# Kernel tuning notes

Hardware: AMD Instinct MI355X
Metric: run time of the kernel (lower is better)

The kernel has to match this reference:

```python
import jax, jax.numpy as jnp
import numpy as np

D_MODEL = 1024
N_HEADS = 16
D_HEAD = D_MODEL // N_HEADS


def setup_inputs() -> dict:
    key = jax.random.key(0)
    k_x, k_wqkv, k_bqkv, k_wo, k_bo = jax.random.split(key, 5)
    B, T = 2, 2048
    scale = 1.0 / np.sqrt(D_MODEL)
    return {
        "x": jax.random.normal(k_x, (B, T, D_MODEL), dtype=jnp.float32),
        "w_qkv": jax.random.uniform(k_wqkv, (D_MODEL, 3 * D_MODEL), jnp.float32, -scale, scale),
        "b_qkv": jax.random.uniform(k_bqkv, (3 * D_MODEL,), jnp.float32, -scale, scale),
        "w_out": jax.random.uniform(k_wo, (D_MODEL, D_MODEL), jnp.float32, -scale, scale),
        "b_out": jax.random.uniform(k_bo, (D_MODEL,), jnp.float32, -scale, scale),
    }


def reference(x, w_qkv, b_qkv, w_out, b_out):
    B, T, D = x.shape
    qkv = x @ w_qkv + b_qkv                      # [B,T,3D]
    q, k, v = jnp.split(qkv, 3, axis=-1)
    # [B,T,D] -> [B,H,T,d]
    def split_heads(t):
        return t.reshape(B, T, N_HEADS, D_HEAD).transpose(0, 2, 1, 3)
    q, k, v = split_heads(q), split_heads(k), split_heads(v)
    scores = jnp.einsum('bhqd,bhkd->bhqk', q, k) / np.sqrt(D_HEAD)
    probs = jax.nn.softmax(scores, axis=-1)      # dropout p=0 (eval)
    out = jnp.einsum('bhqk,bhkd->bhqd', probs, v)
    out = out.transpose(0, 2, 1, 3).reshape(B, T, D)
    return out @ w_out + b_out
```

## Files before the change

kernel.cpp:

```cpp
#include <hip/hip_runtime.h>
#include <hip/hip_bf16.h>
#include <math.h>

#define D_MODEL 1024
#define N_HEADS 16
#define D_HEAD  64
#define SEQ     2048
#define NBATCH  2
#define NROWS   (NBATCH * SEQ)

#define C2F 0.18033688011112042f

typedef __attribute__((ext_vector_type(8))) short short8v;
typedef __attribute__((ext_vector_type(4))) float f32x4;
typedef __attribute__((ext_vector_type(16))) float f32x16;
typedef __attribute__((ext_vector_type(4))) unsigned int u32x4;

__device__ __forceinline__ unsigned short f2bf(float x) {
    unsigned int u = __float_as_uint(x);
    return (unsigned short)((u + 0x7FFFu + ((u >> 16) & 1u)) >> 16);
}
__device__ __forceinline__ void split_bf(float x, unsigned short& hi, unsigned short& lo) {
    unsigned int u = __float_as_uint(x);
    unsigned int ht = u & 0xFFFF0000u;
    hi = (unsigned short)(ht >> 16);
    lo = f2bf(x - __uint_as_float(ht));
}
__device__ __forceinline__ unsigned int cvtpk(float lo, float hi) {
    unsigned int r;
    asm("v_cvt_pk_bf16_f32 %0, %1, %2" : "=v"(r) : "v"(lo), "v"(hi));
    return r;
}
__device__ __forceinline__ short8v u2s(u32x4 v) {
    union { u32x4 u; short8v s; } c; c.u = v; return c.s;
}

__global__ __launch_bounds__(256) void splitT_kernel(
    const float* __restrict__ W, unsigned short* __restrict__ Th,
    unsigned short* __restrict__ Tl, int K, int N, int qcols, int write_lo)
{
    __shared__ float tile[64][68];
    const int tid = threadIdx.x;
    const int nbn = N >> 6;
    const int k0 = (blockIdx.x / nbn) << 6;
    const int n0 = (blockIdx.x % nbn) << 6;
    const int r  = tid >> 4;
    const int c4 = (tid & 15) * 4;

#pragma unroll
    for (int i = 0; i < 4; ++i) {
        float4 v = *(const float4*)(W + (size_t)(k0 + r + i * 16) * N + n0 + c4);
        *(float4*)&tile[r + i * 16][c4] = v;
    }
    __syncthreads();

    const int kl = (tid & 15) * 4;
#pragma unroll
    for (int i = 0; i < 4; ++i) {
        const int nl = (tid >> 4) + i * 16;
        const float sc = (n0 + nl < qcols) ? C2F : 1.0f;
        if (write_lo) {
            ushort4 h4, l4;
            unsigned short h, l;
            split_bf(tile[kl + 0][nl] * sc, h, l); h4.x = h; l4.x = l;
            split_bf(tile[kl + 1][nl] * sc, h, l); h4.y = h; l4.y = l;
            split_bf(tile[kl + 2][nl] * sc, h, l); h4.z = h; l4.z = l;
            split_bf(tile[kl + 3][nl] * sc, h, l); h4.w = h; l4.w = l;
            *(ushort4*)(Th + (size_t)(n0 + nl) * K + k0 + kl) = h4;
            *(ushort4*)(Tl + (size_t)(n0 + nl) * K + k0 + kl) = l4;
        } else {
            ushort4 h4;
            h4.x = f2bf(tile[kl + 0][nl] * sc);
            h4.y = f2bf(tile[kl + 1][nl] * sc);
            h4.z = f2bf(tile[kl + 2][nl] * sc);
            h4.w = f2bf(tile[kl + 3][nl] * sc);
            *(ushort4*)(Th + (size_t)(n0 + nl) * K + k0 + kl) = h4;
        }
    }
}

#define ASTRIDE 40

__global__ __launch_bounds__(256) void gemm_xw_kernel(
    const float* __restrict__ A,
    const unsigned short* __restrict__ Bth,
    const float* __restrict__ bias,
    unsigned short* __restrict__ C, int M, int N, int K, int qcols)
{
    __shared__ __align__(16) unsigned short Ab[128][ASTRIDE];
    __shared__ __align__(16) unsigned short Bh[128][ASTRIDE];

    const int tid  = threadIdx.x;
    const int wave = tid >> 6;
    const int lane = tid & 63;
    const int col  = lane & 15;
    const int q4   = lane >> 4;
    const int wm   = (wave >> 1) * 64;
    const int wn   = (wave & 1) * 64;

    const int nwg = gridDim.x;
    const int cpx = nwg >> 3;
    const int swz = (blockIdx.x & 7) * cpx + (blockIdx.x >> 3);
    const int nbn = N / 128;
    const int bm = (swz / nbn) * 128;
    const int bn = (swz % nbn) * 128;

    const int sr = tid >> 1;
    const int sq = (tid & 1) * 16;
    const float* aptr = A + (size_t)(bm + sr) * K + sq;
    const unsigned short* bhp = Bth + (size_t)(bn + sr) * K + sq;

    f32x4 acc[4][4];
#pragma unroll
    for (int i = 0; i < 4; ++i)
#pragma unroll
        for (int j = 0; j < 4; ++j) acc[i][j] = (f32x4){0.f, 0.f, 0.f, 0.f};

    float4 a0, a1, a2, a3;
    short8v b0h, b1h;

#define G1LOAD(k0) { \
    a0 = *(const float4*)(aptr + (k0)); \
    a1 = *(const float4*)(aptr + (k0) + 4); \
    a2 = *(const float4*)(aptr + (k0) + 8); \
    a3 = *(const float4*)(aptr + (k0) + 12); \
    b0h = *(const short8v*)(bhp + (k0)); \
    b1h = *(const short8v*)(bhp + (k0) + 8); \
}

#define G1WRITE() { \
    u32x4 p0, p1; \
    p0.x = cvtpk(a0.x, a0.y); p0.y = cvtpk(a0.z, a0.w); \
    p0.z = cvtpk(a1.x, a1.y); p0.w = cvtpk(a1.z, a1.w); \
    p1.x = cvtpk(a2.x, a2.y); p1.y = cvtpk(a2.z, a2.w); \
    p1.z = cvtpk(a3.x, a3.y); p1.w = cvtpk(a3.z, a3.w); \
    *(u32x4*)&Ab[sr][sq]     = p0; \
    *(u32x4*)&Ab[sr][sq + 8] = p1; \
    *(short8v*)&Bh[sr][sq]     = b0h; \
    *(short8v*)&Bh[sr][sq + 8] = b1h; \
}

#define G1COMP() { \
    short8v af[4]; \
    _Pragma("unroll") \
    for (int mt = 0; mt < 4; ++mt) \
        af[mt] = *(const short8v*)&Ab[wm + mt * 16 + col][q4 * 8]; \
    _Pragma("unroll") \
    for (int nt = 0; nt < 4; ++nt) { \
        short8v bhf = *(const short8v*)&Bh[wn + nt * 16 + col][q4 * 8]; \
        _Pragma("unroll") \
        for (int mt = 0; mt < 4; ++mt) \
            acc[mt][nt] = __builtin_amdgcn_mfma_f32_16x16x32_bf16(af[mt], bhf, acc[mt][nt], 0, 0, 0); \
    } \
}

    G1LOAD(0);
    G1WRITE();
    for (int k0 = 32; k0 < K; k0 += 32) {
        G1LOAD(k0);
        __syncthreads();
        G1COMP();
        __syncthreads();
        G1WRITE();
    }
    __syncthreads();
    G1COMP();
#undef G1LOAD
#undef G1WRITE
#undef G1COMP

    const float bscale = (bn < qcols) ? C2F : 1.0f;
    float bv[4];
#pragma unroll
    for (int nt = 0; nt < 4; ++nt) bv[nt] = bias[bn + wn + nt * 16 + col] * bscale;

#pragma unroll
    for (int mt = 0; mt < 4; ++mt)
#pragma unroll
        for (int r = 0; r < 4; ++r) {
            const int row = bm + wm + mt * 16 + q4 * 4 + r;
#pragma unroll
            for (int nt = 0; nt < 4; ++nt)
                C[(size_t)row * N + bn + wn + nt * 16 + col] = f2bf(acc[mt][nt][r] + bv[nt]);
        }
}

__global__ __launch_bounds__(256) void gemm_ao_kernel(
    const unsigned short* __restrict__ Aoh,
    const unsigned short* __restrict__ Aol,
    const unsigned short* __restrict__ Bth,
    const unsigned short* __restrict__ Btl,
    const float* __restrict__ bias,
    float* __restrict__ C, int M, int N, int K)
{
    __shared__ __align__(16) unsigned short Ah[128][ASTRIDE];
    __shared__ __align__(16) unsigned short Al[128][ASTRIDE];
    __shared__ __align__(16) unsigned short Bh[128][ASTRIDE];
    __shared__ __align__(16) unsigned short Bl[128][ASTRIDE];

    const int tid  = threadIdx.x;
    const int wave = tid >> 6;
    const int lane = tid & 63;
    const int col  = lane & 15;
    const int q4   = lane >> 4;
    const int wm   = (wave >> 1) * 64;
    const int wn   = (wave & 1) * 64;

    const int nwg = gridDim.x;
    const int cpx = nwg >> 3;
    const int swz = (blockIdx.x & 7) * cpx + (blockIdx.x >> 3);
    const int nbn = N / 128;
    const int bm = (swz / nbn) * 128;
    const int bn = (swz % nbn) * 128;

    const int sr = tid >> 1;
    const int sq = (tid & 1) * 16;
    const unsigned short* ahp = Aoh + (size_t)(bm + sr) * K + sq;
    const unsigned short* alp = Aol + (size_t)(bm + sr) * K + sq;
    const unsigned short* bhp = Bth + (size_t)(bn + sr) * K + sq;
    const unsigned short* blp = Btl + (size_t)(bn + sr) * K + sq;

    f32x4 acc[4][4];
#pragma unroll
    for (int i = 0; i < 4; ++i)
#pragma unroll
        for (int j = 0; j < 4; ++j) acc[i][j] = (f32x4){0.f, 0.f, 0.f, 0.f};

    short8v a0h, a1h, a0l, a1l, b0h, b1h, b0l, b1l;

#define G2LOAD(k0) { \
    a0h = *(const short8v*)(ahp + (k0)); \
    a1h = *(const short8v*)(ahp + (k0) + 8); \
    a0l = *(const short8v*)(alp + (k0)); \
    a1l = *(const short8v*)(alp + (k0) + 8); \
    b0h = *(const short8v*)(bhp + (k0)); \
    b1h = *(const short8v*)(bhp + (k0) + 8); \
    b0l = *(const short8v*)(blp + (k0)); \
    b1l = *(const short8v*)(blp + (k0) + 8); \
}

#define G2WRITE() { \
    *(short8v*)&Ah[sr][sq]     = a0h; \
    *(short8v*)&Ah[sr][sq + 8] = a1h; \
    *(short8v*)&Al[sr][sq]     = a0l; \
    *(short8v*)&Al[sr][sq + 8] = a1l; \
    *(short8v*)&Bh[sr][sq]     = b0h; \
    *(short8v*)&Bh[sr][sq + 8] = b1h; \
    *(short8v*)&Bl[sr][sq]     = b0l; \
    *(short8v*)&Bl[sr][sq + 8] = b1l; \
}

#define G2COMP() { \
    short8v ahf[4], alf[4]; \
    _Pragma("unroll") \
    for (int mt = 0; mt < 4; ++mt) { \
        ahf[mt] = *(const short8v*)&Ah[wm + mt * 16 + col][q4 * 8]; \
        alf[mt] = *(const short8v*)&Al[wm + mt * 16 + col][q4 * 8]; \
    } \
    _Pragma("unroll") \
    for (int nt = 0; nt < 4; ++nt) { \
        short8v bhf = *(const short8v*)&Bh[wn + nt * 16 + col][q4 * 8]; \
        short8v blf = *(const short8v*)&Bl[wn + nt * 16 + col][q4 * 8]; \
        _Pragma("unroll") \
        for (int mt = 0; mt < 4; ++mt) { \
            acc[mt][nt] = __builtin_amdgcn_mfma_f32_16x16x32_bf16(ahf[mt], bhf, acc[mt][nt], 0, 0, 0); \
            acc[mt][nt] = __builtin_amdgcn_mfma_f32_16x16x32_bf16(alf[mt], bhf, acc[mt][nt], 0, 0, 0); \
            acc[mt][nt] = __builtin_amdgcn_mfma_f32_16x16x32_bf16(ahf[mt], blf, acc[mt][nt], 0, 0, 0); \
        } \
    } \
}

    G2LOAD(0);
    G2WRITE();
    for (int k0 = 32; k0 < K; k0 += 32) {
        G2LOAD(k0);
        __syncthreads();
        G2COMP();
        __syncthreads();
        G2WRITE();
    }
    __syncthreads();
    G2COMP();
#undef G2LOAD
#undef G2WRITE
#undef G2COMP

    float bv[4];
#pragma unroll
    for (int nt = 0; nt < 4; ++nt) bv[nt] = bias[bn + wn + nt * 16 + col];

#pragma unroll
    for (int mt = 0; mt < 4; ++mt)
#pragma unroll
        for (int r = 0; r < 4; ++r) {
            const int row = bm + wm + mt * 16 + q4 * 4 + r;
#pragma unroll
            for (int nt = 0; nt < 4; ++nt)
                C[(size_t)row * N + bn + wn + nt * 16 + col] = acc[mt][nt][r] + bv[nt];
        }
}

__global__ __launch_bounds__(256) void attn_mfma_kernel(
    const unsigned short* __restrict__ qkv,
    unsigned short* __restrict__ aoh, unsigned short* __restrict__ aol)
{
    __shared__ __align__(16) unsigned short Ks[64 * 64];
    __shared__ __align__(16) unsigned short Vt[64 * 64];

    const int tid  = threadIdx.x;
    const int wave = tid >> 6;
    const int lane = tid & 63;
    const int l31  = lane & 31;
    const int lh   = lane >> 5;

    const int bh = blockIdx.x;
    const int qt = blockIdx.y;
    const int b = bh >> 4;
    const int h = bh & 15;
    const int qrow0 = b * SEQ + qt * 128 + wave * 32;
    const int krow0 = b * SEQ;

    bool s1;
    {
        int ta = lane, tb = 4096 + lane;
        asm volatile("v_permlane32_swap_b32 %0, %1" : "+v"(ta), "+v"(tb));
        s1 = __all((lane < 32) ? (ta == lane) : (ta == 4096 + lane - 32));
    }

    short8v qf[4];
    {
        const unsigned short* qsrc = qkv + (size_t)(qrow0 + l31) * (3 * D_MODEL) + h * 64 + lh * 8;
#pragma unroll
        for (int s = 0; s < 4; ++s)
            qf[s] = *(const short8v*)(qsrc + s * 16);
    }

    const int krow = tid >> 2;
    const int koff = (tid & 3) * 16;
    const int vk0  = (tid & 31) * 2;
    const int vd0  = (tid >> 5) * 8;

    const unsigned short* kp = qkv + (size_t)(krow0 + krow) * (3 * D_MODEL)
                               + D_MODEL + h * 64 + koff;
    const unsigned short* vp = qkv + (size_t)(krow0 + vk0) * (3 * D_MODEL)
                               + 2 * D_MODEL + h * 64 + vd0;
    const ptrdiff_t CSTRIDE = (ptrdiff_t)64 * 3 * D_MODEL;

    f32x16 ot0, ot1;
#pragma unroll
    for (int r = 0; r < 16; ++r) { ot0[r] = 0.f; ot1[r] = 0.f; }
    float ll = 0.f;

    short8v kg[2], vg[2];
    const int swr = (l31 & 7) << 3;

#define PLSWAP(a, b) asm volatile("v_permlane32_swap_b32 %0, %1" : "+v"(a), "+v"(b))

#define ALOAD() { \
    kg[0] = ((const short8v*)kp)[0]; \
    kg[1] = ((const short8v*)kp)[1]; \
    vg[0] = *(const short8v*)(vp); \
    vg[1] = *(const short8v*)(vp + 3 * D_MODEL); \
    kp += CSTRIDE; vp += CSTRIDE; \
}

#define AWRITE() { \
    const int base = krow * 64 + koff; \
    const int sw = (krow & 7) << 3; \
    *(short8v*)&Ks[(base)     ^ sw] = kg[0]; \
    *(short8v*)&Ks[(base + 8) ^ sw] = kg[1]; \
    _Pragma("unroll") \
    for (int j = 0; j < 8; ++j) { \
        ushort2 w; \
        w.x = ((const unsigned short*)&vg[0])[j]; \
        w.y = ((const unsigned short*)&vg[1])[j]; \
        const int d = vd0 + j; \
        *(ushort2*)&Vt[(d * 64 + vk0) ^ ((d & 7) << 3)] = w; \
    } \
}

#define ACOMPUTE() { \
    f32x16 st0, st1; \
    _Pragma("unroll") for (int r = 0; r < 16; ++r) { st0[r] = 0.f; st1[r] = 0.f; } \
    _Pragma("unroll") \
    for (int s = 0; s < 4; ++s) { \
        short8v kf0 = *(const short8v*)&Ks[(l31 * 64 + s * 16 + lh * 8) ^ swr]; \
        st0 = __builtin_amdgcn_mfma_f32_32x32x16_bf16(kf0, qf[s], st0, 0, 0, 0); \
    } \
    _Pragma("unroll") \
    for (int s = 0; s < 4; ++s) { \
        short8v kf1 = *(const short8v*)&Ks[((32 + l31) * 64 + s * 16 + lh * 8) ^ swr]; \
        st1 = __builtin_amdgcn_mfma_f32_32x32x16_bf16(kf1, qf[s], st1, 0, 0, 0); \
    } \
    _Pragma("unroll") \
    for (int r = 0; r < 16; ++r) { \
        st0[r] = __builtin_exp2f(st0[r]); \
        st1[r] = __builtin_exp2f(st1[r]); \
    } \
    { \
        float a0 = (st0[0] + st0[1]) + (st0[2] + st0[3]); \
        float a1 = (st0[4] + st0[5]) + (st0[6] + st0[7]); \
        float a2 = (st0[8] + st0[9]) + (st0[10] + st0[11]); \
        float a3 = (st0[12] + st0[13]) + (st0[14] + st0[15]); \
        float b0 = (st1[0] + st1[1]) + (st1[2] + st1[3]); \
        float b1 = (st1[4] + st1[5]) + (st1[6] + st1[7]); \
        float b2 = (st1[8] + st1[9]) + (st1[10] + st1[11]); \
        float b3 = (st1[12] + st1[13]) + (st1[14] + st1[15]); \
        float rs = ((a0 + a1) + (a2 + a3)) + ((b0 + b1) + (b2 + b3)); \
        rs += __shfl_xor(rs, 32); \
        ll += rs; \
    } \
    unsigned int pk[16]; \
    _Pragma("unroll") \
    for (int i2 = 0; i2 < 8; ++i2) { \
        pk[i2]     = cvtpk(st0[2 * i2], st0[2 * i2 + 1]); \
        pk[8 + i2] = cvtpk(st1[2 * i2], st1[2 * i2 + 1]); \
    } \
    if (s1) { \
        PLSWAP(pk[0], pk[2]);   PLSWAP(pk[1], pk[3]); \
        PLSWAP(pk[4], pk[6]);   PLSWAP(pk[5], pk[7]); \
        PLSWAP(pk[8], pk[10]);  PLSWAP(pk[9], pk[11]); \
        PLSWAP(pk[12], pk[14]); PLSWAP(pk[13], pk[15]); \
    } else { \
        PLSWAP(pk[2], pk[0]);   PLSWAP(pk[3], pk[1]); \
        PLSWAP(pk[6], pk[4]);   PLSWAP(pk[7], pk[5]); \
        PLSWAP(pk[10], pk[8]);  PLSWAP(pk[11], pk[9]); \
        PLSWAP(pk[14], pk[12]); PLSWAP(pk[15], pk[13]); \
    } \
    u32x4 pf[4]; \
    pf[0].x = pk[0];  pf[0].y = pk[1];  pf[0].z = pk[2];  pf[0].w = pk[3]; \
    pf[1].x = pk[4];  pf[1].y = pk[5];  pf[1].z = pk[6];  pf[1].w = pk[7]; \
    pf[2].x = pk[8];  pf[2].y = pk[9];  pf[2].z = pk[10]; pf[2].w = pk[11]; \
    pf[3].x = pk[12]; pf[3].y = pk[13]; pf[3].z = pk[14]; pf[3].w = pk[15]; \
    _Pragma("unroll") \
    for (int ks2 = 0; ks2 < 4; ++ks2) { \
        const short8v pfr = u2s(pf[ks2]); \
        const int keyoff = ks2 * 16 + lh * 8; \
        short8v vf0 = *(const short8v*)&Vt[(l31 * 64 + keyoff) ^ swr]; \
        ot0 = __builtin_amdgcn_mfma_f32_32x32x16_bf16(vf0, pfr, ot0, 0, 0, 0); \
        short8v vf1 = *(const short8v*)&Vt[((32 + l31) * 64 + keyoff) ^ swr]; \
        ot1 = __builtin_amdgcn_mfma_f32_32x32x16_bf16(vf1, pfr, ot1, 0, 0, 0); \
    } \
}

    ALOAD();
    AWRITE();
    for (int i = 0; i < 31; ++i) {
        ALOAD();
        __syncthreads();
        ACOMPUTE();
        __syncthreads();
        AWRITE();
    }
    __syncthreads();
    ACOMPUTE();
#undef ALOAD
#undef AWRITE
#undef ACOMPUTE
#undef PLSWAP

    const float il = 1.0f / ll;
    const int qrow = qrow0 + l31;
    unsigned short* dh = aoh + (size_t)qrow * D_MODEL + h * 64;
    unsigned short* dl = aol + (size_t)qrow * D_MODEL + h * 64;
#pragma unroll
    for (int r = 0; r < 16; ++r) {
        const int dloc = (r & 3) + 8 * (r >> 2) + 4 * lh;
        unsigned short hh, lo2;
        split_bf(ot0[r] * il, hh, lo2);
        dh[dloc] = hh; dl[dloc] = lo2;
        split_bf(ot1[r] * il, hh, lo2);
        dh[32 + dloc] = hh; dl[32 + dloc] = lo2;
    }
}

extern "C" void kernel_launch(void* const* d_in, const int* in_sizes, int n_in,
                              void* d_out, int out_size, void* d_ws, size_t ws_size,
                              hipStream_t stream) {
    (void)in_sizes; (void)n_in; (void)out_size; (void)ws_size;

    const float* x     = (const float*)d_in[0];
    const float* w_qkv = (const float*)d_in[1];
    const float* b_qkv = (const float*)d_in[2];
    const float* w_out = (const float*)d_in[3];
    const float* b_out = (const float*)d_in[4];
    float* out = (float*)d_out;

    char* ws = (char*)d_ws;
    unsigned short* qkv_bf  = (unsigned short*)(ws);
    unsigned short* aoh     = (unsigned short*)(ws + 25165824);
    unsigned short* aol     = (unsigned short*)(ws + 33554432);
    unsigned short* wqkvT_h = (unsigned short*)(ws + 41943040);
    unsigned short* woutT_h = (unsigned short*)(ws + 48234496);
    unsigned short* woutT_l = (unsigned short*)(ws + 50331648);

    splitT_kernel<<<dim3((D_MODEL / 64) * (3 * D_MODEL / 64)), 256, 0, stream>>>(
        w_qkv, wqkvT_h, (unsigned short*)nullptr, D_MODEL, 3 * D_MODEL, D_MODEL, 0);
    splitT_kernel<<<dim3((D_MODEL / 64) * (D_MODEL / 64)), 256, 0, stream>>>(
        w_out, woutT_h, woutT_l, D_MODEL, D_MODEL, 0, 1);

    gemm_xw_kernel<<<dim3((NROWS / 128) * (3 * D_MODEL / 128)), 256, 0, stream>>>(
        x, wqkvT_h, b_qkv, qkv_bf, NROWS, 3 * D_MODEL, D_MODEL, D_MODEL);

    attn_mfma_kernel<<<dim3(NBATCH * N_HEADS, SEQ / 128), 256, 0, stream>>>(qkv_bf, aoh, aol);

    gemm_ao_kernel<<<dim3((NROWS / 128) * (D_MODEL / 128)), 256, 0, stream>>>(
        aoh, aol, woutT_h, woutT_l, b_out, out, NROWS, D_MODEL, D_MODEL);
}
```

Measured before the change: 155.7 us.

## Split attention over two key halves with a separate merge kernel

The attention kernel gains a third grid dimension that splits the 2048 keys into two halves. Each half writes unnormalized fp32 partial outputs and row sums to workspace, and a new merge kernel adds them, normalizes, and produces the bf16 hi/lo split. This doubles the block count to improve CU occupancy on the attention stage. In exchange it adds about 64MB of extra global traffic, one more launch, and workspace aliasing. The merge is only correct if both halves use the same softmax offset.

```diff
diff --git a/kernel.cpp b/kernel.cpp
--- a/kernel.cpp
+++ b/kernel.cpp
@@ -302,7 +302,8 @@
 
 __global__ __launch_bounds__(256) void attn_mfma_kernel(
     const unsigned short* __restrict__ qkv,
-    unsigned short* __restrict__ aoh, unsigned short* __restrict__ aol)
+    float* __restrict__ Op0, float* __restrict__ Op1,
+    float* __restrict__ l0, float* __restrict__ l1)
 {
     __shared__ __align__(16) unsigned short Ks[64 * 64];
     __shared__ __align__(16) unsigned short Vt[64 * 64];
@@ -315,10 +316,14 @@
 
     const int bh = blockIdx.x;
     const int qt = blockIdx.y;
+    const int ks = blockIdx.z;
     const int b = bh >> 4;
     const int h = bh & 15;
     const int qrow0 = b * SEQ + qt * 128 + wave * 32;
-    const int krow0 = b * SEQ;
+    const int krow0 = b * SEQ + ks * 1024;
+
+    float* __restrict__ Op = ks ? Op1 : Op0;
+    float* __restrict__ lb = ks ? l1 : l0;
 
     bool s1;
     {
@@ -445,7 +450,7 @@
 
     ALOAD();
     AWRITE();
-    for (int i = 0; i < 31; ++i) {
+    for (int i = 0; i < 15; ++i) {
         ALOAD();
         __syncthreads();
         ACOMPUTE();
@@ -459,19 +464,48 @@
 #undef ACOMPUTE
 #undef PLSWAP
 
-    const float il = 1.0f / ll;
     const int qrow = qrow0 + l31;
-    unsigned short* dh = aoh + (size_t)qrow * D_MODEL + h * 64;
-    unsigned short* dl = aol + (size_t)qrow * D_MODEL + h * 64;
+    float* dst = Op + (size_t)qrow * D_MODEL + h * 64;
 #pragma unroll
     for (int r = 0; r < 16; ++r) {
         const int dloc = (r & 3) + 8 * (r >> 2) + 4 * lh;
-        unsigned short hh, lo2;
-        split_bf(ot0[r] * il, hh, lo2);
-        dh[dloc] = hh; dl[dloc] = lo2;
-        split_bf(ot1[r] * il, hh, lo2);
-        dh[32 + dloc] = hh; dl[32 + dloc] = lo2;
-    }
+        dst[dloc]      = ot0[r];
+        dst[32 + dloc] = ot1[r];
+    }
+    if (lh == 0) lb[qrow * N_HEADS + h] = ll;
+}
+
+__global__ __launch_bounds__(256) void merge_kernel(
+    const float* __restrict__ Op0, const float* __restrict__ Op1,
+    const float* __restrict__ l0, const float* __restrict__ l1,
+    unsigned short* __restrict__ aoh, unsigned short* __restrict__ aol)
+{
+    const size_t e0 = ((size_t)blockIdx.x * 256 + threadIdx.x) * 8;
+    const int row = (int)(e0 >> 10);
+    const int col = (int)(e0 & 1023);
+    const int hh  = col >> 6;
+    const float il = 1.0f / (l0[row * N_HEADS + hh] + l1[row * N_HEADS + hh]);
+
+    float4 a0 = *(const float4*)(Op0 + e0);
+    float4 a1 = *(const float4*)(Op0 + e0 + 4);
+    float4 b0 = *(const float4*)(Op1 + e0);
+    float4 b1 = *(const float4*)(Op1 + e0 + 4);
+
+    ushort4 ha, la, hb, lb;
+    unsigned short hi, lo;
+    split_bf((a0.x + b0.x) * il, hi, lo); ha.x = hi; la.x = lo;
+    split_bf((a0.y + b0.y) * il, hi, lo); ha.y = hi; la.y = lo;
+    split_bf((a0.z + b0.z) * il, hi, lo); ha.z = hi; la.z = lo;
+    split_bf((a0.w + b0.w) * il, hi, lo); ha.w = hi; la.w = lo;
+    split_bf((a1.x + b1.x) * il, hi, lo); hb.x = hi; lb.x = lo;
+    split_bf((a1.y + b1.y) * il, hi, lo); hb.y = hi; lb.y = lo;
+    split_bf((a1.z + b1.z) * il, hi, lo); hb.z = hi; lb.z = lo;
+    split_bf((a1.w + b1.w) * il, hi, lo); hb.w = hi; lb.w = lo;
+
+    *(ushort4*)(aoh + e0)     = ha;
+    *(ushort4*)(aoh + e0 + 4) = hb;
+    *(ushort4*)(aol + e0)     = la;
+    *(ushort4*)(aol + e0 + 4) = lb;
 }
 
 extern "C" void kernel_launch(void* const* d_in, const int* in_sizes, int n_in,
@@ -488,11 +522,15 @@
 
     char* ws = (char*)d_ws;
     unsigned short* qkv_bf  = (unsigned short*)(ws);
-    unsigned short* aoh     = (unsigned short*)(ws + 25165824);
-    unsigned short* aol     = (unsigned short*)(ws + 33554432);
-    unsigned short* wqkvT_h = (unsigned short*)(ws + 41943040);
-    unsigned short* woutT_h = (unsigned short*)(ws + 48234496);
-    unsigned short* woutT_l = (unsigned short*)(ws + 50331648);
+    unsigned short* aoh     = (unsigned short*)(ws);
+    unsigned short* aol     = (unsigned short*)(ws + 8388608);
+    float*          Op0     = (float*)(ws + 25165824);
+    unsigned short* wqkvT_h = (unsigned short*)(ws + 25165824);
+    float*          Op1     = (float*)(ws + 41943040);
+    float*          l0      = (float*)(ws + 58720256);
+    float*          l1      = (float*)(ws + 58982400);
+    unsigned short* woutT_h = (unsigned short*)(ws + 59244544);
+    unsigned short* woutT_l = (unsigned short*)(ws + 61341696);
 
     splitT_kernel<<<dim3((D_MODEL / 64) * (3 * D_MODEL / 64)), 256, 0, stream>>>(
         w_qkv, wqkvT_h, (unsigned short*)nullptr, D_MODEL, 3 * D_MODEL, D_MODEL, 0);
@@ -502,7 +540,11 @@
     gemm_xw_kernel<<<dim3((NROWS / 128) * (3 * D_MODEL / 128)), 256, 0, stream>>>(
         x, wqkvT_h, b_qkv, qkv_bf, NROWS, 3 * D_MODEL, D_MODEL, D_MODEL);
 
-    attn_mfma_kernel<<<dim3(NBATCH * N_HEADS, SEQ / 128), 256, 0, stream>>>(qkv_bf, aoh, aol);
+    attn_mfma_kernel<<<dim3(NBATCH * N_HEADS, SEQ / 128, 2), 256, 0, stream>>>(
+        qkv_bf, Op0, Op1, l0, l1);
+
+    merge_kernel<<<dim3(NROWS * D_MODEL / (256 * 8)), 256, 0, stream>>>(
+        Op0, Op1, l0, l1, aoh, aol);
 
     gemm_ao_kernel<<<dim3((NROWS / 128) * (D_MODEL / 128)), 256, 0, stream>>>(
         aoh, aol, woutT_h, woutT_l, b_out, out, NROWS, D_MODEL, D_MODEL);
```

Result: slower. 162.3 us (+4.2%).
